# Kernel optimization log

Measured on AMD Instinct MI355X. Metric: run time of the kernel, lower is better.

## Reference

```python
import jax, jax.numpy as jnp
import numpy as np

B, T, H, NH, K = 8, 1024, 1024, 16, 3
HD = H // NH
EPS = 1e-5


def _ln(x, g, b):
    m = jnp.mean(x, axis=-1, keepdims=True)
    v = jnp.mean((x - m) ** 2, axis=-1, keepdims=True)
    return (x - m) * jax.lax.rsqrt(v + EPS) * g + b


def _ffn(x, g, b, w1, b1, w2, b2):
    h = jax.nn.gelu(_ln(x, g, b) @ w1 + b1, approximate=False)
    return h @ w2 + b2


def setup_inputs() -> dict:
    key = jax.random.key(0)
    ks = jax.random.split(key, 10)
    s = 0.02
    d = {}
    d['x'] = jax.random.normal(ks[0], (B, T, H), jnp.float32)
    d['ln1_g'] = jnp.ones((H,), jnp.float32); d['ln1_b'] = jnp.zeros((H,), jnp.float32)
    d['ffn1_w1'] = jax.random.normal(ks[1], (H, 2 * H), jnp.float32) * s
    d['ffn1_b1'] = jnp.zeros((2 * H,), jnp.float32)
    d['ffn1_w2'] = jax.random.normal(ks[2], (2 * H, H), jnp.float32) * s
    d['ffn1_b2'] = jnp.zeros((H,), jnp.float32)
    d['an_g'] = jnp.ones((H,), jnp.float32); d['an_b'] = jnp.zeros((H,), jnp.float32)
    d['qkv_w'] = jax.random.normal(ks[3], (H, 3 * H), jnp.float32) * s
    d['qkv_b'] = jnp.zeros((3 * H,), jnp.float32)
    d['out_w'] = jax.random.normal(ks[4], (H, H), jnp.float32) * s
    d['out_b'] = jnp.zeros((H,), jnp.float32)
    d['cn_g'] = jnp.ones((H,), jnp.float32); d['cn_b'] = jnp.zeros((H,), jnp.float32)
    d['dw_k'] = jax.random.normal(ks[5], (H, 1, K), jnp.float32) * s  # depthwise [O,I/g,K]
    d['dw_b'] = jnp.zeros((H,), jnp.float32)
    d['pw_w'] = jax.random.normal(ks[6], (H, H), jnp.float32) * s  # pointwise [out,in]
    d['pw_b'] = jnp.zeros((H,), jnp.float32)
    d['ln2_g'] = jnp.ones((H,), jnp.float32); d['ln2_b'] = jnp.zeros((H,), jnp.float32)
    d['ffn2_w1'] = jax.random.normal(ks[7], (H, 2 * H), jnp.float32) * s
    d['ffn2_b1'] = jnp.zeros((2 * H,), jnp.float32)
    d['ffn2_w2'] = jax.random.normal(ks[8], (2 * H, H), jnp.float32) * s
    d['ffn2_b2'] = jnp.zeros((H,), jnp.float32)
    return d


def reference(x, ln1_g, ln1_b, ffn1_w1, ffn1_b1, ffn1_w2, ffn1_b2,
              an_g, an_b, qkv_w, qkv_b, out_w, out_b,
              cn_g, cn_b, dw_k, dw_b, pw_w, pw_b,
              ln2_g, ln2_b, ffn2_w1, ffn2_b1, ffn2_w2, ffn2_b2):
    # macaron FFN 1
    x = x + 0.5 * _ffn(x, ln1_g, ln1_b, ffn1_w1, ffn1_b1, ffn1_w2, ffn1_b2)

    # causal self-attention (pre-norm)
    h = _ln(x, an_g, an_b)
    qkv = (h @ qkv_w + qkv_b).reshape(B, T, 3, NH, HD)
    q, k, v = qkv[:, :, 0], qkv[:, :, 1], qkv[:, :, 2]  # [B,T,NH,HD]
    scale = 1.0 / np.sqrt(HD).astype(np.float32)
    scores = jnp.einsum('bqhd,bkhd->bhqk', q, k) * scale  # [B,NH,T,T]
    causal = jnp.tril(jnp.ones((T, T), dtype=bool))
    scores = jnp.where(causal[None, None], scores, -jnp.inf)
    attn = jax.nn.softmax(scores, axis=-1)
    o = jnp.einsum('bhqk,bkhd->bqhd', attn, v).reshape(B, T, H)
    x = x + (o @ out_w + out_b)

    # conv module: LN -> causal depthwise conv(k=3) -> GELU -> pointwise conv
    c = _ln(x, cn_g, cn_b).transpose(0, 2, 1)  # [B,H,T]
    c = jnp.pad(c, ((0, 0), (0, 0), (K - 1, 0)))  # causal left pad
    c = jax.lax.conv_general_dilated(
        c, dw_k, window_strides=(1,), padding='VALID',
        dimension_numbers=('NCH', 'OIH', 'NCH'), feature_group_count=H)
    c = c + dw_b[None, :, None]
    c = jax.nn.gelu(c, approximate=False)
    c = jnp.einsum('oc,bct->bot', pw_w, c) + pw_b[None, :, None]  # 1x1 conv
    x = x + c.transpose(0, 2, 1)

    # macaron FFN 2
    x = x + 0.5 * _ffn(x, ln2_g, ln2_b, ffn2_w1, ffn2_b1, ffn2_w2, ffn2_b2)
    return x
```

## Files before the change

kernel.cpp:

```cpp
#include <hip/hip_runtime.h>
#include <hip/hip_bf16.h>
#include <math.h>

typedef __bf16 bf16;
typedef __bf16 bf16x8 __attribute__((ext_vector_type(8)));
typedef float  f32x4  __attribute__((ext_vector_type(4)));

#define B_   8
#define T_   1024
#define H_   1024
#define MTOK (B_ * T_)

static __device__ __forceinline__ float gelu_f(float x) {
    return 0.5f * x * (1.0f + erff(x * 0.70710678118654752f));
}

static __device__ __forceinline__ void async16(const bf16* g, bf16* l) {
    __builtin_amdgcn_global_load_lds(
        (const __attribute__((address_space(1))) void*)g,
        (__attribute__((address_space(3))) void*)l, 16, 0, 0);
}

__global__ __launch_bounds__(256)
void transpose_cast_k(const float* __restrict__ in, bf16* __restrict__ out,
                      int Kd, int Nd)
{
    __shared__ float tile[32][33];
    int n0 = blockIdx.x * 32;
    int k0 = blockIdx.y * 32;
    int tx = threadIdx.x & 31, ty = threadIdx.x >> 5;
#pragma unroll
    for (int i = 0; i < 32; i += 8)
        tile[ty + i][tx] = in[(size_t)(k0 + ty + i) * Nd + n0 + tx];
    __syncthreads();
#pragma unroll
    for (int i = 0; i < 32; i += 8)
        out[(size_t)(n0 + ty + i) * Kd + k0 + tx] = (bf16)tile[tx][ty + i];
}

__global__ __launch_bounds__(256)
void cast_k(const float* __restrict__ in, bf16* __restrict__ out)
{
    int i = blockIdx.x * 256 + threadIdx.x;
    float4 v = ((const float4*)in)[i];
    bf16* o = out + (size_t)i * 4;
    o[0] = (bf16)v.x; o[1] = (bf16)v.y; o[2] = (bf16)v.z; o[3] = (bf16)v.w;
}

__global__ __launch_bounds__(256)
void transpose_v_k(const bf16* __restrict__ qkv, bf16* __restrict__ vt)
{
    __shared__ bf16 tile[64][72];
    const int t0 = blockIdx.x * 64;
    const int bh = blockIdx.y;
    const int b = bh >> 4, h = bh & 15;
    const int tid = threadIdx.x;
#pragma unroll
    for (int i = 0; i < 2; i++) {
        int c = tid + i * 256;
        int row = c >> 3, ch = (c & 7) << 3;
        *(bf16x8*)(&tile[row][ch]) =
            *(const bf16x8*)(&qkv[(size_t)(b * T_ + t0 + row) * 3072 + 2048 + h * 64 + ch]);
    }
    __syncthreads();
#pragma unroll
    for (int i = 0; i < 2; i++) {
        int c = tid + i * 256;
        int hd = c >> 3, tc = (c & 7) << 3;
        bf16x8 v;
#pragma unroll
        for (int j = 0; j < 8; j++) v[j] = tile[tc + j][hd];
        *(bf16x8*)(&vt[((size_t)bh * 64 + hd) * T_ + t0 + tc]) = v;
    }
}

__global__ __launch_bounds__(256)
void ln_k(const float* __restrict__ x, const float* __restrict__ g,
          const float* __restrict__ b, bf16* __restrict__ out)
{
    int row = blockIdx.x;
    float4 v = ((const float4*)(x + (size_t)row * H_))[threadIdx.x];
    float s  = v.x + v.y + v.z + v.w;
    float s2 = v.x * v.x + v.y * v.y + v.z * v.z + v.w * v.w;
#pragma unroll
    for (int off = 32; off > 0; off >>= 1) {
        s  += __shfl_down(s, off);
        s2 += __shfl_down(s2, off);
    }
    __shared__ float red[8];
    int wave = threadIdx.x >> 6, lane = threadIdx.x & 63;
    if (lane == 0) { red[wave] = s; red[wave + 4] = s2; }
    __syncthreads();
    s  = red[0] + red[1] + red[2] + red[3];
    s2 = red[4] + red[5] + red[6] + red[7];
    float mean = s * (1.0f / H_);
    float var  = s2 * (1.0f / H_) - mean * mean;
    float rstd = rsqrtf(var + 1e-5f);
    int c = threadIdx.x * 4;
    float4 gv = *(const float4*)(g + c);
    float4 bv = *(const float4*)(b + c);
    bf16* o = out + (size_t)row * H_ + c;
    o[0] = (bf16)((v.x - mean) * rstd * gv.x + bv.x);
    o[1] = (bf16)((v.y - mean) * rstd * gv.y + bv.y);
    o[2] = (bf16)((v.z - mean) * rstd * gv.z + bv.z);
    o[3] = (bf16)((v.w - mean) * rstd * gv.w + bv.w);
}

__global__ __launch_bounds__(256)
void dwconv_k(const bf16* __restrict__ cl, const float* __restrict__ kw,
              const float* __restrict__ kb, bf16* __restrict__ out)
{
    size_t idx = (size_t)blockIdx.x * 256 + threadIdx.x;
    int ch = (int)(idx & (H_ - 1));
    int t  = (int)((idx >> 10) & (T_ - 1));
    float acc = kb[ch];
    float w0 = kw[ch * 3 + 0], w1 = kw[ch * 3 + 1], w2 = kw[ch * 3 + 2];
    acc += (float)cl[idx] * w2;
    if (t >= 1) acc += (float)cl[idx - H_] * w1;
    if (t >= 2) acc += (float)cl[idx - 2 * H_] * w0;
    out[idx] = (bf16)gelu_f(acc);
}

#define BM 128
#define BN 128
#define BK 32

template<int EPI>
__global__ __launch_bounds__(256)
void gemm_k(const bf16* __restrict__ A, const bf16* __restrict__ WT,
            const float* __restrict__ bias, const float* __restrict__ res,
            float* __restrict__ outF, bf16* __restrict__ outB,
            int N, int K)
{
    __shared__ bf16 As[BM * BK];
    __shared__ bf16 Bs[BN * BK];
    const int tid  = threadIdx.x;
    const int wave = tid >> 6;
    const int lane = tid & 63;
    const int quad = lane >> 4;
    const int lr   = lane & 15;
    const int bm = blockIdx.x * BM;
    const int bn = blockIdx.y * BN;
    const int wm = (wave & 1) * 64;
    const int wn = (wave >> 1) * 64;

    const int crow = lane >> 2;
    const int ccol = (lane & 3) << 3;

    f32x4 acc[4][4];
#pragma unroll
    for (int mi = 0; mi < 4; mi++)
#pragma unroll
        for (int ni = 0; ni < 4; ni++)
#pragma unroll
            for (int r = 0; r < 4; r++) acc[mi][ni][r] = 0.f;

    for (int k0 = 0; k0 < K; k0 += BK) {
#pragma unroll
        for (int t = 0; t < 2; t++) {
            const int c = wave * 2 + t;
            async16(&A[(size_t)(bm + c * 16 + crow) * K + k0 + ccol], &As[c * 512]);
            async16(&WT[(size_t)(bn + c * 16 + crow) * K + k0 + ccol], &Bs[c * 512]);
        }
        __syncthreads();
        bf16x8 af[4], bfr[4];
#pragma unroll
        for (int mi = 0; mi < 4; mi++)
            af[mi] = *(const bf16x8*)(&As[(wm + mi * 16 + lr) * BK + quad * 8]);
#pragma unroll
        for (int ni = 0; ni < 4; ni++)
            bfr[ni] = *(const bf16x8*)(&Bs[(wn + ni * 16 + lr) * BK + quad * 8]);
#pragma unroll
        for (int mi = 0; mi < 4; mi++)
#pragma unroll
            for (int ni = 0; ni < 4; ni++)
                acc[mi][ni] = __builtin_amdgcn_mfma_f32_16x16x32_bf16(
                    af[mi], bfr[ni], acc[mi][ni], 0, 0, 0);
        __syncthreads();
    }

#pragma unroll
    for (int mi = 0; mi < 4; mi++) {
#pragma unroll
        for (int ni = 0; ni < 4; ni++) {
            int col = bn + wn + ni * 16 + lr;
            float bv = bias[col];
#pragma unroll
            for (int r = 0; r < 4; r++) {
                int row = bm + wm + mi * 16 + quad * 4 + r;
                size_t idx = (size_t)row * N + col;
                float v = acc[mi][ni][r] + bv;
                if (EPI == 0)      outB[idx] = (bf16)gelu_f(v);
                else if (EPI == 1) outB[idx] = (bf16)v;
                else if (EPI == 2) outF[idx] = v + res[idx];
                else               outF[idx] = res[idx] + 0.5f * v;
            }
        }
    }
}

#define ASTR 72

__global__ __launch_bounds__(256)
void attn_k(const bf16* __restrict__ qkv, const bf16* __restrict__ vt,
            bf16* __restrict__ o)
{
    const int qt = blockIdx.x;
    const int bh = blockIdx.y;
    const int b = bh >> 4, h = bh & 15;
    const int tid  = threadIdx.x;
    const int wave = tid >> 6, lane = tid & 63;
    const int quad = lane >> 4, lr = lane & 15;
    const int wq = wave * 16;

    __shared__ bf16 Qs[64 * ASTR];
    __shared__ bf16 Ks[64 * ASTR];
    __shared__ bf16 Vts[64 * ASTR];
    __shared__ bf16 Ps[4][16 * ASTR];

    const size_t base = (size_t)b * T_ * 3072;
    const size_t vtbase = (size_t)bh * 64 * T_;

#pragma unroll
    for (int i = 0; i < 2; i++) {
        int c = tid + i * 256;
        int row = c >> 3, ch = (c & 7) << 3;
        *(bf16x8*)(&Qs[row * ASTR + ch]) =
            *(const bf16x8*)(&qkv[base + (size_t)(qt * 64 + row) * 3072 + h * 64 + ch]);
    }
    __syncthreads();
    bf16x8 qf[2];
    qf[0] = *(const bf16x8*)(&Qs[(wq + lr) * ASTR + quad * 8]);
    qf[1] = *(const bf16x8*)(&Qs[(wq + lr) * ASTR + 32 + quad * 8]);

    f32x4 oacc[4];
    float m_run[4], l_run[4];
#pragma unroll
    for (int ni = 0; ni < 4; ni++)
#pragma unroll
        for (int r = 0; r < 4; r++) oacc[ni][r] = 0.f;
#pragma unroll
    for (int r = 0; r < 4; r++) { m_run[r] = -INFINITY; l_run[r] = 0.f; }

    for (int kt = 0; kt <= qt; kt++) {
        __syncthreads();
#pragma unroll
        for (int i = 0; i < 2; i++) {
            int c = tid + i * 256;
            int row = c >> 3, ch = (c & 7) << 3;
            *(bf16x8*)(&Ks[row * ASTR + ch]) =
                *(const bf16x8*)(&qkv[base + (size_t)(kt * 64 + row) * 3072 + 1024 + h * 64 + ch]);
            *(bf16x8*)(&Vts[row * ASTR + ch]) =
                *(const bf16x8*)(&vt[vtbase + (size_t)row * T_ + kt * 64 + ch]);
        }
        __syncthreads();

        f32x4 sv[4];
#pragma unroll
        for (int ni = 0; ni < 4; ni++) {
            bf16x8 kf0 = *(const bf16x8*)(&Ks[(ni * 16 + lr) * ASTR + quad * 8]);
            bf16x8 kf1 = *(const bf16x8*)(&Ks[(ni * 16 + lr) * ASTR + 32 + quad * 8]);
            f32x4 t;
#pragma unroll
            for (int r = 0; r < 4; r++) t[r] = 0.f;
            t = __builtin_amdgcn_mfma_f32_16x16x32_bf16(qf[0], kf0, t, 0, 0, 0);
            t = __builtin_amdgcn_mfma_f32_16x16x32_bf16(qf[1], kf1, t, 0, 0, 0);
            sv[ni] = t;
        }

        const int gq_base = qt * 64 + wq + quad * 4;
        const int gs_base = kt * 64 + lr;
        float rmax[4];
#pragma unroll
        for (int r = 0; r < 4; r++) rmax[r] = -INFINITY;
#pragma unroll
        for (int ni = 0; ni < 4; ni++)
#pragma unroll
            for (int r = 0; r < 4; r++) {
                float xv = sv[ni][r] * 0.125f;
                if (gs_base + ni * 16 > gq_base + r) xv = -INFINITY;
                sv[ni][r] = xv;
                rmax[r] = fmaxf(rmax[r], xv);
            }
#pragma unroll
        for (int off = 1; off < 16; off <<= 1)
#pragma unroll
            for (int r = 0; r < 4; r++)
                rmax[r] = fmaxf(rmax[r], __shfl_xor(rmax[r], off));

        float alpha[4], rsum[4];
#pragma unroll
        for (int r = 0; r < 4; r++) {
            float mn = fmaxf(m_run[r], rmax[r]);
            alpha[r] = __expf(m_run[r] - mn);
            m_run[r] = mn;
            rsum[r] = 0.f;
        }
#pragma unroll
        for (int ni = 0; ni < 4; ni++)
#pragma unroll
            for (int r = 0; r < 4; r++) {
                float p = __expf(sv[ni][r] - m_run[r]);
                rsum[r] += p;
                Ps[wave][(quad * 4 + r) * ASTR + ni * 16 + lr] = (bf16)p;
            }
#pragma unroll
        for (int off = 1; off < 16; off <<= 1)
#pragma unroll
            for (int r = 0; r < 4; r++)
                rsum[r] += __shfl_xor(rsum[r], off);
#pragma unroll
        for (int r = 0; r < 4; r++)
            l_run[r] = l_run[r] * alpha[r] + rsum[r];
#pragma unroll
        for (int ni = 0; ni < 4; ni++)
#pragma unroll
            for (int r = 0; r < 4; r++)
                oacc[ni][r] *= alpha[r];

        bf16x8 pf0 = *(const bf16x8*)(&Ps[wave][lr * ASTR + quad * 8]);
        bf16x8 pf1 = *(const bf16x8*)(&Ps[wave][lr * ASTR + 32 + quad * 8]);
#pragma unroll
        for (int ni = 0; ni < 4; ni++) {
            bf16x8 vf0 = *(const bf16x8*)(&Vts[(ni * 16 + lr) * ASTR + quad * 8]);
            bf16x8 vf1 = *(const bf16x8*)(&Vts[(ni * 16 + lr) * ASTR + 32 + quad * 8]);
            oacc[ni] = __builtin_amdgcn_mfma_f32_16x16x32_bf16(pf0, vf0, oacc[ni], 0, 0, 0);
            oacc[ni] = __builtin_amdgcn_mfma_f32_16x16x32_bf16(pf1, vf1, oacc[ni], 0, 0, 0);
        }
    }

#pragma unroll
    for (int r = 0; r < 4; r++) {
        float inv = 1.0f / l_run[r];
        int gq = qt * 64 + wq + quad * 4 + r;
#pragma unroll
        for (int ni = 0; ni < 4; ni++)
            o[((size_t)(b * T_ + gq)) * H_ + h * 64 + ni * 16 + lr] =
                (bf16)(oacc[ni][r] * inv);
    }
}

extern "C" void kernel_launch(void* const* d_in, const int* in_sizes, int n_in,
                              void* d_out, int out_size, void* d_ws, size_t ws_size,
                              hipStream_t stream)
{
    const float* x_in  = (const float*)d_in[0];
    const float* ln1_g = (const float*)d_in[1];
    const float* ln1_b = (const float*)d_in[2];
    const float* f1w1  = (const float*)d_in[3];
    const float* f1b1  = (const float*)d_in[4];
    const float* f1w2  = (const float*)d_in[5];
    const float* f1b2  = (const float*)d_in[6];
    const float* an_g  = (const float*)d_in[7];
    const float* an_b  = (const float*)d_in[8];
    const float* qkv_w = (const float*)d_in[9];
    const float* qkv_b = (const float*)d_in[10];
    const float* out_w = (const float*)d_in[11];
    const float* out_b = (const float*)d_in[12];
    const float* cn_g  = (const float*)d_in[13];
    const float* cn_b  = (const float*)d_in[14];
    const float* dw_k  = (const float*)d_in[15];
    const float* dw_b  = (const float*)d_in[16];
    const float* pw_w  = (const float*)d_in[17];
    const float* pw_b  = (const float*)d_in[18];
    const float* ln2_g = (const float*)d_in[19];
    const float* ln2_b = (const float*)d_in[20];
    const float* f2w1  = (const float*)d_in[21];
    const float* f2b1  = (const float*)d_in[22];
    const float* f2w2  = (const float*)d_in[23];
    const float* f2b2  = (const float*)d_in[24];
    float* outp = (float*)d_out;

    char* ws = (char*)d_ws;
    size_t off = 0;
    auto alloc = [&](size_t bytes) {
        char* p = ws + off;
        off += (bytes + 255) & ~(size_t)255;
        return p;
    };
    bf16* w1T_1 = (bf16*)alloc(2048ULL * 1024 * 2);
    bf16* w2T_1 = (bf16*)alloc(1024ULL * 2048 * 2);
    bf16* qkvT  = (bf16*)alloc(3072ULL * 1024 * 2);
    bf16* outT  = (bf16*)alloc(1024ULL * 1024 * 2);
    bf16* pwB   = (bf16*)alloc(1024ULL * 1024 * 2);
    bf16* w1T_2 = (bf16*)alloc(2048ULL * 1024 * 2);
    bf16* w2T_2 = (bf16*)alloc(1024ULL * 2048 * 2);
    bf16* bufa  = (bf16*)alloc((size_t)MTOK * 1024 * 2);
    bf16* gbuf  = (bf16*)alloc((size_t)MTOK * 1024 * 2);
    bf16* hid   = (bf16*)alloc((size_t)MTOK * 3072 * 2);
    float* xw   = (float*)alloc((size_t)MTOK * 1024 * 4);
    bf16* vt    = gbuf;

    transpose_cast_k<<<dim3(64, 32), 256, 0, stream>>>(f1w1, w1T_1, 1024, 2048);
    transpose_cast_k<<<dim3(32, 64), 256, 0, stream>>>(f1w2, w2T_1, 2048, 1024);
    transpose_cast_k<<<dim3(96, 32), 256, 0, stream>>>(qkv_w, qkvT, 1024, 3072);
    transpose_cast_k<<<dim3(32, 32), 256, 0, stream>>>(out_w, outT, 1024, 1024);
    transpose_cast_k<<<dim3(64, 32), 256, 0, stream>>>(f2w1, w1T_2, 1024, 2048);
    transpose_cast_k<<<dim3(32, 64), 256, 0, stream>>>(f2w2, w2T_2, 2048, 1024);
    cast_k<<<1024, 256, 0, stream>>>(pw_w, pwB);

    ln_k<<<MTOK, 256, 0, stream>>>(x_in, ln1_g, ln1_b, bufa);
    gemm_k<0><<<dim3(64, 16), 256, 0, stream>>>(bufa, w1T_1, f1b1, nullptr, nullptr, hid, 2048, 1024);
    gemm_k<3><<<dim3(64, 8), 256, 0, stream>>>(hid, w2T_1, f1b2, x_in, xw, nullptr, 1024, 2048);

    ln_k<<<MTOK, 256, 0, stream>>>(xw, an_g, an_b, bufa);
    gemm_k<1><<<dim3(64, 24), 256, 0, stream>>>(bufa, qkvT, qkv_b, nullptr, nullptr, hid, 3072, 1024);
    transpose_v_k<<<dim3(16, 128), 256, 0, stream>>>(hid, vt);
    attn_k<<<dim3(16, 128), 256, 0, stream>>>(hid, vt, bufa);
    gemm_k<2><<<dim3(64, 8), 256, 0, stream>>>(bufa, outT, out_b, xw, xw, nullptr, 1024, 1024);

    ln_k<<<MTOK, 256, 0, stream>>>(xw, cn_g, cn_b, bufa);
    dwconv_k<<<MTOK * 1024 / 256, 256, 0, stream>>>(bufa, dw_k, dw_b, gbuf);
    gemm_k<2><<<dim3(64, 8), 256, 0, stream>>>(gbuf, pwB, pw_b, xw, xw, nullptr, 1024, 1024);

    ln_k<<<MTOK, 256, 0, stream>>>(xw, ln2_g, ln2_b, bufa);
    gemm_k<0><<<dim3(64, 16), 256, 0, stream>>>(bufa, w1T_2, f2b1, nullptr, nullptr, hid, 2048, 1024);
    gemm_k<3><<<dim3(64, 8), 256, 0, stream>>>(hid, w2T_2, f2b2, xw, outp, nullptr, 1024, 2048);
}
```

Baseline: 743.7 us.

## Unroll GEMM K-loop to 64 and load attention K/V directly into registers

The GEMM now loads two 32-wide K slices per barrier pair, halving the number of __syncthreads per unit of K work. The attention kernel drops its shared-memory staging of Q, K and V: each wave reads its MFMA fragments straight from global memory, which removes the block-wide barriers in the key loop but repeats K/V loads across the four waves. Q is prescaled by 0.125 in bf16, which adds a small rounding difference. The causal mask is applied only on the diagonal tile.

```diff
diff --git a/kernel.cpp b/kernel.cpp
--- a/kernel.cpp
+++ b/kernel.cpp
@@ -123,7 +123,6 @@
 
 #define BM 128
 #define BN 128
-#define BK 32
 
 template<int EPI>
 __global__ __launch_bounds__(256)
@@ -132,8 +131,8 @@
             float* __restrict__ outF, bf16* __restrict__ outB,
             int N, int K)
 {
-    __shared__ bf16 As[BM * BK];
-    __shared__ bf16 Bs[BN * BK];
+    __shared__ bf16 As[2][BM * 32];
+    __shared__ bf16 Bs[2][BN * 32];
     const int tid  = threadIdx.x;
     const int wave = tid >> 6;
     const int lane = tid & 63;
@@ -155,27 +154,35 @@
 #pragma unroll
             for (int r = 0; r < 4; r++) acc[mi][ni][r] = 0.f;
 
-    for (int k0 = 0; k0 < K; k0 += BK) {
-#pragma unroll
-        for (int t = 0; t < 2; t++) {
-            const int c = wave * 2 + t;
-            async16(&A[(size_t)(bm + c * 16 + crow) * K + k0 + ccol], &As[c * 512]);
-            async16(&WT[(size_t)(bn + c * 16 + crow) * K + k0 + ccol], &Bs[c * 512]);
+    for (int k0 = 0; k0 < K; k0 += 64) {
+#pragma unroll
+        for (int half = 0; half < 2; half++) {
+#pragma unroll
+            for (int t = 0; t < 2; t++) {
+                const int c = wave * 2 + t;
+                async16(&A[(size_t)(bm + c * 16 + crow) * K + k0 + half * 32 + ccol],
+                        &As[half][c * 512]);
+                async16(&WT[(size_t)(bn + c * 16 + crow) * K + k0 + half * 32 + ccol],
+                        &Bs[half][c * 512]);
+            }
         }
         __syncthreads();
-        bf16x8 af[4], bfr[4];
-#pragma unroll
-        for (int mi = 0; mi < 4; mi++)
-            af[mi] = *(const bf16x8*)(&As[(wm + mi * 16 + lr) * BK + quad * 8]);
-#pragma unroll
-        for (int ni = 0; ni < 4; ni++)
-            bfr[ni] = *(const bf16x8*)(&Bs[(wn + ni * 16 + lr) * BK + quad * 8]);
-#pragma unroll
-        for (int mi = 0; mi < 4; mi++)
+#pragma unroll
+        for (int half = 0; half < 2; half++) {
+            bf16x8 af[4], bfr[4];
+#pragma unroll
+            for (int mi = 0; mi < 4; mi++)
+                af[mi] = *(const bf16x8*)(&As[half][(wm + mi * 16 + lr) * 32 + quad * 8]);
 #pragma unroll
             for (int ni = 0; ni < 4; ni++)
-                acc[mi][ni] = __builtin_amdgcn_mfma_f32_16x16x32_bf16(
-                    af[mi], bfr[ni], acc[mi][ni], 0, 0, 0);
+                bfr[ni] = *(const bf16x8*)(&Bs[half][(wn + ni * 16 + lr) * 32 + quad * 8]);
+#pragma unroll
+            for (int mi = 0; mi < 4; mi++)
+#pragma unroll
+                for (int ni = 0; ni < 4; ni++)
+                    acc[mi][ni] = __builtin_amdgcn_mfma_f32_16x16x32_bf16(
+                        af[mi], bfr[ni], acc[mi][ni], 0, 0, 0);
+        }
         __syncthreads();
     }
 
@@ -211,27 +218,18 @@
     const int tid  = threadIdx.x;
     const int wave = tid >> 6, lane = tid & 63;
     const int quad = lane >> 4, lr = lane & 15;
-    const int wq = wave * 16;
-
-    __shared__ bf16 Qs[64 * ASTR];
-    __shared__ bf16 Ks[64 * ASTR];
-    __shared__ bf16 Vts[64 * ASTR];
+
     __shared__ bf16 Ps[4][16 * ASTR];
 
-    const size_t base = (size_t)b * T_ * 3072;
-    const size_t vtbase = (size_t)bh * 64 * T_;
-
-#pragma unroll
-    for (int i = 0; i < 2; i++) {
-        int c = tid + i * 256;
-        int row = c >> 3, ch = (c & 7) << 3;
-        *(bf16x8*)(&Qs[row * ASTR + ch]) =
-            *(const bf16x8*)(&qkv[base + (size_t)(qt * 64 + row) * 3072 + h * 64 + ch]);
-    }
-    __syncthreads();
-    bf16x8 qf[2];
-    qf[0] = *(const bf16x8*)(&Qs[(wq + lr) * ASTR + quad * 8]);
-    qf[1] = *(const bf16x8*)(&Qs[(wq + lr) * ASTR + 32 + quad * 8]);
+    const int gq0 = qt * 64 + wave * 16;
+    const size_t qrow = ((size_t)(b * T_ + gq0 + lr)) * 3072 + h * 64;
+    bf16x8 qf0 = *(const bf16x8*)(&qkv[qrow + quad * 8]);
+    bf16x8 qf1 = *(const bf16x8*)(&qkv[qrow + 32 + quad * 8]);
+#pragma unroll
+    for (int j = 0; j < 8; j++) {
+        qf0[j] = (bf16)((float)qf0[j] * 0.125f);
+        qf1[j] = (bf16)((float)qf1[j] * 0.125f);
+    }
 
     f32x4 oacc[4];
     float m_run[4], l_run[4];
@@ -242,46 +240,55 @@
 #pragma unroll
     for (int r = 0; r < 4; r++) { m_run[r] = -INFINITY; l_run[r] = 0.f; }
 
+    const size_t kbase = (size_t)b * T_ * 3072 + 1024 + h * 64;
+    const size_t vbase = (size_t)bh * 64 * T_;
+
     for (int kt = 0; kt <= qt; kt++) {
-        __syncthreads();
-#pragma unroll
-        for (int i = 0; i < 2; i++) {
-            int c = tid + i * 256;
-            int row = c >> 3, ch = (c & 7) << 3;
-            *(bf16x8*)(&Ks[row * ASTR + ch]) =
-                *(const bf16x8*)(&qkv[base + (size_t)(kt * 64 + row) * 3072 + 1024 + h * 64 + ch]);
-            *(bf16x8*)(&Vts[row * ASTR + ch]) =
-                *(const bf16x8*)(&vt[vtbase + (size_t)row * T_ + kt * 64 + ch]);
-        }
-        __syncthreads();
-
+        bf16x8 kf[4][2];
+#pragma unroll
+        for (int ni = 0; ni < 4; ni++) {
+            const bf16* kp = &qkv[kbase + (size_t)(kt * 64 + ni * 16 + lr) * 3072];
+            kf[ni][0] = *(const bf16x8*)(kp + quad * 8);
+            kf[ni][1] = *(const bf16x8*)(kp + 32 + quad * 8);
+        }
         f32x4 sv[4];
 #pragma unroll
         for (int ni = 0; ni < 4; ni++) {
-            bf16x8 kf0 = *(const bf16x8*)(&Ks[(ni * 16 + lr) * ASTR + quad * 8]);
-            bf16x8 kf1 = *(const bf16x8*)(&Ks[(ni * 16 + lr) * ASTR + 32 + quad * 8]);
             f32x4 t;
 #pragma unroll
             for (int r = 0; r < 4; r++) t[r] = 0.f;
-            t = __builtin_amdgcn_mfma_f32_16x16x32_bf16(qf[0], kf0, t, 0, 0, 0);
-            t = __builtin_amdgcn_mfma_f32_16x16x32_bf16(qf[1], kf1, t, 0, 0, 0);
+            t = __builtin_amdgcn_mfma_f32_16x16x32_bf16(qf0, kf[ni][0], t, 0, 0, 0);
+            t = __builtin_amdgcn_mfma_f32_16x16x32_bf16(qf1, kf[ni][1], t, 0, 0, 0);
             sv[ni] = t;
         }
 
-        const int gq_base = qt * 64 + wq + quad * 4;
-        const int gs_base = kt * 64 + lr;
+        bf16x8 vf[4][2];
+#pragma unroll
+        for (int ni = 0; ni < 4; ni++) {
+            const bf16* vp = &vt[vbase + (size_t)(ni * 16 + lr) * T_ + kt * 64];
+            vf[ni][0] = *(const bf16x8*)(vp + quad * 8);
+            vf[ni][1] = *(const bf16x8*)(vp + 32 + quad * 8);
+        }
+
         float rmax[4];
 #pragma unroll
         for (int r = 0; r < 4; r++) rmax[r] = -INFINITY;
-#pragma unroll
-        for (int ni = 0; ni < 4; ni++)
-#pragma unroll
-            for (int r = 0; r < 4; r++) {
-                float xv = sv[ni][r] * 0.125f;
-                if (gs_base + ni * 16 > gq_base + r) xv = -INFINITY;
-                sv[ni][r] = xv;
-                rmax[r] = fmaxf(rmax[r], xv);
-            }
+        if (kt == qt) {
+#pragma unroll
+            for (int ni = 0; ni < 4; ni++)
+#pragma unroll
+                for (int r = 0; r < 4; r++) {
+                    if (kt * 64 + ni * 16 + lr > gq0 + quad * 4 + r)
+                        sv[ni][r] = -INFINITY;
+                    rmax[r] = fmaxf(rmax[r], sv[ni][r]);
+                }
+        } else {
+#pragma unroll
+            for (int ni = 0; ni < 4; ni++)
+#pragma unroll
+                for (int r = 0; r < 4; r++)
+                    rmax[r] = fmaxf(rmax[r], sv[ni][r]);
+        }
 #pragma unroll
         for (int off = 1; off < 16; off <<= 1)
 #pragma unroll
@@ -322,17 +329,15 @@
         bf16x8 pf1 = *(const bf16x8*)(&Ps[wave][lr * ASTR + 32 + quad * 8]);
 #pragma unroll
         for (int ni = 0; ni < 4; ni++) {
-            bf16x8 vf0 = *(const bf16x8*)(&Vts[(ni * 16 + lr) * ASTR + quad * 8]);
-            bf16x8 vf1 = *(const bf16x8*)(&Vts[(ni * 16 + lr) * ASTR + 32 + quad * 8]);
-            oacc[ni] = __builtin_amdgcn_mfma_f32_16x16x32_bf16(pf0, vf0, oacc[ni], 0, 0, 0);
-            oacc[ni] = __builtin_amdgcn_mfma_f32_16x16x32_bf16(pf1, vf1, oacc[ni], 0, 0, 0);
+            oacc[ni] = __builtin_amdgcn_mfma_f32_16x16x32_bf16(pf0, vf[ni][0], oacc[ni], 0, 0, 0);
+            oacc[ni] = __builtin_amdgcn_mfma_f32_16x16x32_bf16(pf1, vf[ni][1], oacc[ni], 0, 0, 0);
         }
     }
 
 #pragma unroll
     for (int r = 0; r < 4; r++) {
         float inv = 1.0f / l_run[r];
-        int gq = qt * 64 + wq + quad * 4 + r;
+        int gq = gq0 + quad * 4 + r;
 #pragma unroll
         for (int ni = 0; ni < 4; ni++)
             o[((size_t)(b * T_ + gq)) * H_ + h * 64 + ni * 16 + lr] =
```

New measurement: 808.4 us. 8.7% more time.
